# Kernel tuning notes

Hardware: AMD Instinct MI355X
Metric: run time of the kernel (lower is better)

## Reference

```python
import jax, jax.numpy as jnp
import numpy as np

N_NODES = 100_000
N_EDGES = 1_600_000
N_GRAPHS = 1_000
VOCAB = 65
D_IN = 128
D_HID = 128


def setup_inputs() -> dict:
    key = jax.random.key(0)
    ks = jax.random.split(key, 12)
    x = jax.random.randint(ks[0], (N_NODES,), 0, VOCAB)
    edge_index = jax.random.randint(ks[1], (2, N_EDGES), 0, N_NODES)
    batch = jnp.sort(jax.random.randint(ks[2], (N_NODES,), 0, N_GRAPHS))

    def lin(k, fan_in, fan_out):
        bound = 1.0 / np.sqrt(fan_in)
        kw, kb = jax.random.split(k)
        W = jax.random.uniform(kw, (fan_in, fan_out), jnp.float32, -bound, bound)
        b = jax.random.uniform(kb, (fan_out,), jnp.float32, -bound, bound)
        return W, b

    emb = jax.random.normal(ks[3], (VOCAB, D_IN), jnp.float32)
    W1, b1 = lin(ks[4], D_IN, D_HID)
    W2, b2 = lin(ks[5], D_HID, D_HID)
    W3, b3 = lin(ks[6], D_HID, D_HID)
    Wf, bf = lin(ks[7], D_HID, 1)
    return {"x": x, "edge_index": edge_index, "batch": batch, "emb": emb,
            "W1": W1, "b1": b1, "W2": W2, "b2": b2, "W3": W3, "b3": b3,
            "Wf": Wf, "bf": bf}


def gcn_conv(h, W, b, src, dst, n):
    # PyG GCNConv: add self-loops, symmetric normalization D^-1/2 A_hat D^-1/2,
    # transform then aggregate messages at dst.
    h = h @ W                                             # [N, H]
    deg = jnp.zeros((n,), h.dtype).at[dst].add(1.0) + 1.0  # self-loop adds 1
    dinv = jax.lax.rsqrt(deg)                             # [N]
    coef = dinv[src] * dinv[dst]                          # [E]
    agg = jax.ops.segment_sum(h[src] * coef[:, None], dst, num_segments=n)
    return agg + h * (dinv * dinv)[:, None] + b           # self-loop term + bias


def reference(x, edge_index, batch, emb, W1, b1, W2, b2, W3, b3, Wf, bf):
    # Embedding with max_norm=1: renormalize looked-up rows to norm <= 1.
    e = emb[x]                                            # [N, D_IN]
    nrm = jnp.linalg.norm(e, axis=-1, keepdims=True)
    e = e * jnp.minimum(1.0, 1.0 / jnp.maximum(nrm, 1e-7))

    src, dst = edge_index[0], edge_index[1]
    h = jax.nn.relu(gcn_conv(e, W1, b1, src, dst, N_NODES))
    h = jax.nn.relu(gcn_conv(h, W2, b2, src, dst, N_NODES))
    h = jax.nn.relu(gcn_conv(h, W3, b3, src, dst, N_NODES))

    g = jax.ops.segment_max(h, batch, num_segments=N_GRAPHS)  # [G, H]
    return (g @ Wf + bf).ravel()                               # [G]
```

## Files before the change

### kernel.cpp

```cpp
#include <hip/hip_runtime.h>
#include <hip/hip_bf16.h>

#define N_NODES  100000
#define N_EDGES  1600000
#define N_GRAPHS 1000
#define D        128
#define CAP      64
#define NBKT     256
#define N_BUCKETS ((N_NODES + NBKT - 1) / NBKT)
#define HWGS     256
#define EPW      ((N_EDGES + HWGS - 1) / HWGS)

typedef __attribute__((ext_vector_type(8))) short bf16x8;
typedef __attribute__((ext_vector_type(4))) float f32x4;

__device__ inline f32x4 mfma16(bf16x8 a, bf16x8 b, f32x4 c) {
    return __builtin_amdgcn_mfma_f32_16x16x32_bf16(a, b, c, 0, 0, 0);
}

__device__ inline unsigned short f2bf(float f) {
    unsigned u = __float_as_uint(f);
    unsigned r = u + 0x7fffu + ((u >> 16) & 1u);
    return (unsigned short)(r >> 16);
}

__global__ __launch_bounds__(256) void k_hist(const int* __restrict__ dst,
                                              int* __restrict__ bcnt,
                                              int* __restrict__ wgoff,
                                              const float* __restrict__ W1,
                                              const float* __restrict__ W2,
                                              const float* __restrict__ W3,
                                              short* __restrict__ frag) {
    int w = blockIdx.x, t = threadIdx.x;
    if (w >= HWGS) {
        int L = w - HWGS;
        const float* W = (L == 0) ? W1 : (L == 1) ? W2 : W3;
        short* fh = frag + (size_t)L * 32768;
        short* fl = fh + 16384;
        #pragma unroll
        for (int f = 0; f < 8; f++) {
            int id = t + f * 256;
            int lane = id & 63, kb = (id >> 6) & 3, nt = id >> 8;
            int k0 = kb * 32 + (lane >> 4) * 8;
            int n  = nt * 16 + (lane & 15);
            bf16x8 vh, vl;
            #pragma unroll
            for (int j = 0; j < 8; j++) {
                float wv = W[(k0 + j) * 128 + n];
                unsigned short hs = f2bf(wv);
                float hf = __uint_as_float((unsigned)hs << 16);
                vh[j] = (short)hs;
                vl[j] = (short)f2bf(wv - hf);
            }
            *(bf16x8*)&fh[id * 8] = vh;
            *(bf16x8*)&fl[id * 8] = vl;
        }
        return;
    }
    __shared__ int hist[N_BUCKETS];
    for (int b = t; b < N_BUCKETS; b += 256) hist[b] = 0;
    __syncthreads();
    int e0 = w * EPW, e1 = min(e0 + EPW, N_EDGES);
    for (int i = e0 + t; i < e1; i += 256)
        atomicAdd(&hist[dst[i] >> 8], 1);
    __syncthreads();
    for (int b = t; b < N_BUCKETS; b += 256) {
        int h = hist[b];
        wgoff[w * N_BUCKETS + b] = h ? atomicAdd(&bcnt[b], h) : 0;
    }
}

__global__ __launch_bounds__(512) void k_bscan(const int* __restrict__ bcnt,
                                               int* __restrict__ boff) {
    __shared__ int s[512];
    int t = threadIdx.x;
    int v = (t < N_BUCKETS) ? bcnt[t] : 0;
    s[t] = v;
    __syncthreads();
    for (int off = 1; off < 512; off <<= 1) {
        int val = (t >= off) ? s[t - off] : 0;
        __syncthreads();
        s[t] += val;
        __syncthreads();
    }
    if (t < N_BUCKETS) boff[t] = s[t] - v;
    if (t == 0) boff[N_BUCKETS] = N_EDGES;
}

__global__ __launch_bounds__(256) void k_scat(const int* __restrict__ src,
                                              const int* __restrict__ dst,
                                              const int* __restrict__ boff,
                                              const int* __restrict__ wgoff,
                                              int* __restrict__ ep) {
    __shared__ int cnt[N_BUCKETS];
    int t = threadIdx.x, w = blockIdx.x;
    for (int b = t; b < N_BUCKETS; b += 256) cnt[b] = 0;
    __syncthreads();
    int e0 = w * EPW, e1 = min(e0 + EPW, N_EDGES);
    for (int i = e0 + t; i < e1; i += 256) {
        int d = dst[i], b = d >> 8;
        int r = atomicAdd(&cnt[b], 1);
        ep[boff[b] + wgoff[w * N_BUCKETS + b] + r] = (src[i] << 8) | (d & 255);
    }
}

__global__ __launch_bounds__(256) void k_ell(const int* __restrict__ ep,
                                             const int* __restrict__ boff,
                                             int* __restrict__ ell,
                                             int* __restrict__ fill) {
    __shared__ int cnt_s[NBKT];
    __shared__ int ell_s[NBKT * CAP];
    int t = threadIdx.x, b = blockIdx.x;
    int nb0 = b * NBKT;
    int nn = min(NBKT, N_NODES - nb0);
    for (int i = t; i < NBKT; i += 256) cnt_s[i] = 0;
    __syncthreads();
    int e0 = boff[b], e1 = boff[b + 1];
    for (int i = e0 + t; i < e1; i += 256) {
        int e = ep[i];
        int ln = e & 255;
        int r = atomicAdd(&cnt_s[ln], 1);
        if (r < CAP) ell_s[ln * CAP + r] = (int)((unsigned)e >> 8);
    }
    __syncthreads();
    for (int i = t; i < nn * CAP; i += 256)
        ell[(size_t)nb0 * CAP + i] = ell_s[i];
    if (t < nn) fill[nb0 + t] = cnt_s[t];
}

__global__ __launch_bounds__(256) void k_embed(const int* __restrict__ x,
                                               const float* __restrict__ emb,
                                               unsigned short* __restrict__ h,
                                               const int* __restrict__ batch,
                                               int* __restrict__ gstart,
                                               int* __restrict__ gend) {
    int gid = blockIdx.x * 256 + threadIdx.x;
    if (gid < N_NODES) {
        int b = batch[gid];
        if (gid == 0 || batch[gid - 1] != b) gstart[b] = gid;
        if (gid == N_NODES - 1 || batch[gid + 1] != b) gend[b] = gid + 1;
    }
    int n = blockIdx.x * 4 + (threadIdx.x >> 6);
    int lane = threadIdx.x & 63;
    if (n >= N_NODES) return;
    int xi = x[n];
    float2 v = ((const float2*)(emb + (size_t)xi * D))[lane];
    float ss = v.x * v.x + v.y * v.y;
    #pragma unroll
    for (int off = 32; off; off >>= 1) ss += __shfl_xor(ss, off);
    float nrm = sqrtf(ss);
    float scale = fminf(1.0f, 1.0f / fmaxf(nrm, 1e-7f));
    unsigned pk = (unsigned)f2bf(v.x * scale) | ((unsigned)f2bf(v.y * scale) << 16);
    ((unsigned*)(h + (size_t)n * D))[lane] = pk;
}

__global__ __launch_bounds__(256) void k_gemm(const unsigned short* __restrict__ A,
                                              const short* __restrict__ frag,
                                              const int* __restrict__ fill,
                                              unsigned short* __restrict__ Cb) {
    __shared__ short Bf[16384];
    int t = threadIdx.x;
    int w = t >> 6, lane = t & 63;
    int quad = lane >> 4, col = lane & 15;
    size_t r0 = (size_t)blockIdx.x * 128 + w * 32;

    bf16x8 a0[4], a1[4];
    #pragma unroll
    for (int kb = 0; kb < 4; kb++) {
        a0[kb] = *(const bf16x8*)&A[(r0 + col)      * D + kb * 32 + quad * 8];
        a1[kb] = *(const bf16x8*)&A[(r0 + 16 + col) * D + kb * 32 + quad * 8];
    }
    f32x4 acc[2][8];
    #pragma unroll
    for (int r = 0; r < 2; r++)
        #pragma unroll
        for (int n = 0; n < 8; n++) acc[r][n] = (f32x4){0.f, 0.f, 0.f, 0.f};

    #pragma unroll
    for (int half = 0; half < 2; half++) {
        __syncthreads();
        {
            const int4* g4 = (const int4*)(frag + half * 16384);
            int4* l4 = (int4*)Bf;
            #pragma unroll
            for (int i = 0; i < 8; i++) l4[t + i * 256] = g4[t + i * 256];
        }
        __syncthreads();
        #pragma unroll
        for (int kb = 0; kb < 4; kb++)
            #pragma unroll
            for (int nt = 0; nt < 8; nt++) {
                bf16x8 b = *(const bf16x8*)&Bf[((nt * 4 + kb) * 64 + lane) * 8];
                acc[0][nt] = mfma16(a0[kb], b, acc[0][nt]);
                acc[1][nt] = mfma16(a1[kb], b, acc[1][nt]);
            }
    }
    #pragma unroll
    for (int r = 0; r < 2; r++) {
        size_t row = r0 + r * 16 + quad * 4;
        #pragma unroll
        for (int g = 0; g < 4; g++) {
            float dv = (row + g < N_NODES)
                         ? 1.0f / sqrtf((float)fill[row + g] + 1.0f) : 0.f;
            #pragma unroll
            for (int nt = 0; nt < 8; nt++)
                Cb[(row + g) * D + nt * 16 + col] = f2bf(acc[r][nt][g] * dv);
        }
    }
}

__device__ inline void acc8(float* acc, int4 r) {
    unsigned u0 = (unsigned)r.x, u1 = (unsigned)r.y,
             u2 = (unsigned)r.z, u3 = (unsigned)r.w;
    acc[0] += __uint_as_float(u0 << 16);
    acc[1] += __uint_as_float(u0 & 0xffff0000u);
    acc[2] += __uint_as_float(u1 << 16);
    acc[3] += __uint_as_float(u1 & 0xffff0000u);
    acc[4] += __uint_as_float(u2 << 16);
    acc[5] += __uint_as_float(u2 & 0xffff0000u);
    acc[6] += __uint_as_float(u3 << 16);
    acc[7] += __uint_as_float(u3 & 0xffff0000u);
}

#define LOADGRP(R, S, IT)                                                    \
    {                                                                        \
        _Pragma("unroll")                                                    \
        for (int k = 0; k < 4; k++) {                                        \
            int s = __shfl((S), (IT) * 16 + k * 4 + quad);                   \
            R[k] = *(const int4*)&hw2[((unsigned)s << 7) + cOff];            \
        }                                                                    \
    }
#define ACCGRP(A, R)                                                         \
    {                                                                        \
        _Pragma("unroll")                                                    \
        for (int k = 0; k < 4; k++) acc8((A), R[k]);                         \
    }

__global__ __launch_bounds__(256) void k_agg(const unsigned short* __restrict__ hw2,
                                             unsigned short* __restrict__ hout,
                                             const int* __restrict__ fill,
                                             const int* __restrict__ ell,
                                             const float* __restrict__ bias) {
    int w = threadIdx.x >> 6, lane = threadIdx.x & 63;
    int na = blockIdx.x * 8 + w * 2;
    int nb = na + 1;
    if (na >= N_NODES) return;
    int quad = lane >> 4;
    int l16  = lane & 15;
    unsigned cOff = (unsigned)(l16 << 3);

    int fa = __builtin_amdgcn_readfirstlane(fill[na]);
    int fb = __builtin_amdgcn_readfirstlane(fill[nb]);
    int ca = min(fa, CAP), cb = min(fb, CAP);
    int sa = (lane < ca) ? ell[na * CAP + lane] : N_NODES;
    int sb = (lane < cb) ? ell[nb * CAP + lane] : N_NODES;
    int ia = (ca + 15) >> 4; ia += (ia == 0);
    int ib = (cb + 15) >> 4; ib += (ib == 0);

    float accA[8], accB[8];
    #pragma unroll
    for (int c = 0; c < 8; c++) { accA[c] = 0.f; accB[c] = 0.f; }

    int4 A0[4], A1[4], B0[4], B1[4];
    LOADGRP(A0, sa, 0);
    LOADGRP(B0, sb, 0);
    if (1 < ia) LOADGRP(A1, sa, 1);
    ACCGRP(accA, A0);
    if (1 < ib) LOADGRP(B1, sb, 1);
    ACCGRP(accB, B0);
    if (ia > 1 || ib > 1) {
        if (2 < ia) LOADGRP(A0, sa, 2);
        if (1 < ia) ACCGRP(accA, A1);
        if (2 < ib) LOADGRP(B0, sb, 2);
        if (1 < ib) ACCGRP(accB, B1);
        if (ia > 2 || ib > 2) {
            if (3 < ia) LOADGRP(A1, sa, 3);
            if (2 < ia) ACCGRP(accA, A0);
            if (3 < ib) LOADGRP(B1, sb, 3);
            if (2 < ib) ACCGRP(accB, B0);
            if (3 < ia) ACCGRP(accA, A1);
            if (3 < ib) ACCGRP(accB, B1);
        }
    }

    #pragma unroll
    for (int c = 0; c < 8; c++) {
        accA[c] += __shfl_xor(accA[c], 16);
        accA[c] += __shfl_xor(accA[c], 32);
        accB[c] += __shfl_xor(accB[c], 16);
        accB[c] += __shfl_xor(accB[c], 32);
    }
    if (quad < 2) {
        int   n   = quad ? nb : na;
        int   fr  = quad ? fb : fa;
        float* acc = quad ? accB : accA;
        int4 sr = *(const int4*)&hw2[((unsigned)n << 7) + cOff];
        acc8(acc, sr);
        float di = 1.0f / sqrtf((float)fr + 1.0f);
        float4 bA = *(const float4*)&bias[l16 * 8];
        float4 bB = *(const float4*)&bias[l16 * 8 + 4];
        float o[8];
        o[0] = fmaxf(acc[0] * di + bA.x, 0.f);
        o[1] = fmaxf(acc[1] * di + bA.y, 0.f);
        o[2] = fmaxf(acc[2] * di + bA.z, 0.f);
        o[3] = fmaxf(acc[3] * di + bA.w, 0.f);
        o[4] = fmaxf(acc[4] * di + bB.x, 0.f);
        o[5] = fmaxf(acc[5] * di + bB.y, 0.f);
        o[6] = fmaxf(acc[6] * di + bB.z, 0.f);
        o[7] = fmaxf(acc[7] * di + bB.w, 0.f);
        int4 pk;
        pk.x = (int)((unsigned)f2bf(o[0]) | ((unsigned)f2bf(o[1]) << 16));
        pk.y = (int)((unsigned)f2bf(o[2]) | ((unsigned)f2bf(o[3]) << 16));
        pk.z = (int)((unsigned)f2bf(o[4]) | ((unsigned)f2bf(o[5]) << 16));
        pk.w = (int)((unsigned)f2bf(o[6]) | ((unsigned)f2bf(o[7]) << 16));
        *(int4*)&hout[((unsigned)n << 7) + cOff] = pk;
    }
}

__global__ __launch_bounds__(256) void k_pool(const unsigned short* __restrict__ h,
                                              const int* __restrict__ gstart,
                                              const int* __restrict__ gend,
                                              const float* __restrict__ Wf,
                                              const float* __restrict__ bf,
                                              float* __restrict__ out) {
    __shared__ float2 sm[4][64];
    int g = blockIdx.x;
    int w = threadIdx.x >> 6, lane = threadIdx.x & 63;
    int s = gstart[g], e = gend[g];
    float2 m = make_float2(-3.402823466e38f, -3.402823466e38f);
    for (int i = s + w; i < e; i += 4) {
        unsigned u = ((const unsigned*)(h + (size_t)i * D))[lane];
        m.x = fmaxf(m.x, __uint_as_float(u << 16));
        m.y = fmaxf(m.y, __uint_as_float(u & 0xffff0000u));
    }
    sm[w][lane] = m;
    __syncthreads();
    if (w == 0) {
        float2 a = sm[0][lane], b2 = sm[1][lane], c = sm[2][lane], d = sm[3][lane];
        m.x = fmaxf(fmaxf(a.x, b2.x), fmaxf(c.x, d.x));
        m.y = fmaxf(fmaxf(a.y, b2.y), fmaxf(c.y, d.y));
        float2 wf = ((const float2*)Wf)[lane];
        float val = m.x * wf.x + m.y * wf.y;
        #pragma unroll
        for (int off = 32; off; off >>= 1) val += __shfl_xor(val, off);
        if (lane == 0) out[g] = val + bf[0];
    }
}

extern "C" void kernel_launch(void* const* d_in, const int* in_sizes, int n_in,
                              void* d_out, int out_size, void* d_ws, size_t ws_size,
                              hipStream_t stream) {
    const int*   x    = (const int*)d_in[0];
    const int*   ei   = (const int*)d_in[1];
    const int*   batch= (const int*)d_in[2];
    const float* emb  = (const float*)d_in[3];
    const float* W1   = (const float*)d_in[4];
    const float* b1   = (const float*)d_in[5];
    const float* W2   = (const float*)d_in[6];
    const float* b2   = (const float*)d_in[7];
    const float* W3   = (const float*)d_in[8];
    const float* b3   = (const float*)d_in[9];
    const float* Wf   = (const float*)d_in[10];
    const float* bf   = (const float*)d_in[11];
    float* out = (float*)d_out;

    const int* src = ei;
    const int* dst = ei + N_EDGES;

    char* p = (char*)d_ws;
    unsigned short* hAb  = (unsigned short*)p; p += (size_t)(N_NODES + 128) * D * 2;
    unsigned short* hwb  = (unsigned short*)p; p += (size_t)(N_NODES + 128) * D * 2;
    int*            ep   = (int*)hwb;
    int*   fill     = (int*)p;              p += (size_t)N_NODES * 4;
    int*   gbounds  = (int*)p;              p += (size_t)2 * N_GRAPHS * 4;
    int*   ell      = (int*)p;              p += (size_t)N_NODES * CAP * 4;
    int*   wgoff    = (int*)p;              p += (size_t)HWGS * N_BUCKETS * 4;
    int*   bcnt     = (int*)p;              p += (size_t)(N_BUCKETS + 4) * 4;
    int*   boff     = (int*)p;              p += (size_t)(N_BUCKETS + 4) * 4;
    short* wfrag    = (short*)p;            p += (size_t)3 * 32768 * 2;
    (void)p;
    int* gstart = gbounds;
    int* gend   = gbounds + N_GRAPHS;

    hipMemsetAsync(bcnt, 0, (size_t)N_BUCKETS * 4, stream);
    hipMemsetAsync(gbounds, 0x7f, (size_t)2 * N_GRAPHS * 4, stream);

    const int NW = (N_NODES + 3) / 4;
    const int GB = (N_NODES + 127) / 128;
    const int AB = N_NODES / 8;

    k_hist <<<HWGS + 3, 256, 0, stream>>>(dst, bcnt, wgoff, W1, W2, W3, wfrag);
    k_bscan<<<1, 512, 0, stream>>>(bcnt, boff);
    k_scat <<<HWGS, 256, 0, stream>>>(src, dst, boff, wgoff, ep);
    k_ell  <<<N_BUCKETS, 256, 0, stream>>>(ep, boff, ell, fill);

    k_embed<<<NW, 256, 0, stream>>>(x, emb, hAb, batch, gstart, gend);

    k_gemm<<<GB, 256, 0, stream>>>(hAb, wfrag,         fill, hwb);
    k_agg <<<AB, 256, 0, stream>>>(hwb, hAb, fill, ell, b1);
    k_gemm<<<GB, 256, 0, stream>>>(hAb, wfrag + 32768, fill, hwb);
    k_agg <<<AB, 256, 0, stream>>>(hwb, hAb, fill, ell, b2);
    k_gemm<<<GB, 256, 0, stream>>>(hAb, wfrag + 65536, fill, hwb);
    k_agg <<<AB, 256, 0, stream>>>(hwb, hAb, fill, ell, b3);

    k_pool<<<N_GRAPHS, 256, 0, stream>>>(hAb, gstart, gend, Wf, bf, out);
}
```

Before: 413.6 us.

## Fuse embedding lookup into first GEMM and move graph bounds into hist kernel

```diff
diff --git a/kernel.cpp b/kernel.cpp
--- a/kernel.cpp
+++ b/kernel.cpp
@@ -10,6 +10,7 @@
 #define N_BUCKETS ((N_NODES + NBKT - 1) / NBKT)
 #define HWGS     256
 #define EPW      ((N_EDGES + HWGS - 1) / HWGS)
+#define BNDB     ((N_NODES + 255) / 256)
 
 typedef __attribute__((ext_vector_type(8))) short bf16x8;
 typedef __attribute__((ext_vector_type(4))) float f32x4;
@@ -30,8 +31,20 @@
                                               const float* __restrict__ W1,
                                               const float* __restrict__ W2,
                                               const float* __restrict__ W3,
-                                              short* __restrict__ frag) {
+                                              short* __restrict__ frag,
+                                              const int* __restrict__ batch,
+                                              int* __restrict__ gstart,
+                                              int* __restrict__ gend) {
     int w = blockIdx.x, t = threadIdx.x;
+    if (w >= HWGS + 3) {
+        int gid = (w - HWGS - 3) * 256 + t;
+        if (gid < N_NODES) {
+            int b = batch[gid];
+            if (gid == 0 || batch[gid - 1] != b) gstart[b] = gid;
+            if (gid == N_NODES - 1 || batch[gid + 1] != b) gend[b] = gid + 1;
+        }
+        return;
+    }
     if (w >= HWGS) {
         int L = w - HWGS;
         const float* W = (L == 0) ? W1 : (L == 1) ? W2 : W3;
@@ -128,73 +141,25 @@
     if (t < nn) fill[nb0 + t] = cnt_s[t];
 }
 
-__global__ __launch_bounds__(256) void k_embed(const int* __restrict__ x,
-                                               const float* __restrict__ emb,
-                                               unsigned short* __restrict__ h,
-                                               const int* __restrict__ batch,
-                                               int* __restrict__ gstart,
-                                               int* __restrict__ gend) {
-    int gid = blockIdx.x * 256 + threadIdx.x;
-    if (gid < N_NODES) {
-        int b = batch[gid];
-        if (gid == 0 || batch[gid - 1] != b) gstart[b] = gid;
-        if (gid == N_NODES - 1 || batch[gid + 1] != b) gend[b] = gid + 1;
-    }
-    int n = blockIdx.x * 4 + (threadIdx.x >> 6);
-    int lane = threadIdx.x & 63;
-    if (n >= N_NODES) return;
-    int xi = x[n];
-    float2 v = ((const float2*)(emb + (size_t)xi * D))[lane];
-    float ss = v.x * v.x + v.y * v.y;
-    #pragma unroll
-    for (int off = 32; off; off >>= 1) ss += __shfl_xor(ss, off);
-    float nrm = sqrtf(ss);
-    float scale = fminf(1.0f, 1.0f / fmaxf(nrm, 1e-7f));
-    unsigned pk = (unsigned)f2bf(v.x * scale) | ((unsigned)f2bf(v.y * scale) << 16);
-    ((unsigned*)(h + (size_t)n * D))[lane] = pk;
-}
-
-__global__ __launch_bounds__(256) void k_gemm(const unsigned short* __restrict__ A,
-                                              const short* __restrict__ frag,
-                                              const int* __restrict__ fill,
-                                              unsigned short* __restrict__ Cb) {
-    __shared__ short Bf[16384];
-    int t = threadIdx.x;
-    int w = t >> 6, lane = t & 63;
-    int quad = lane >> 4, col = lane & 15;
-    size_t r0 = (size_t)blockIdx.x * 128 + w * 32;
-
-    bf16x8 a0[4], a1[4];
-    #pragma unroll
-    for (int kb = 0; kb < 4; kb++) {
-        a0[kb] = *(const bf16x8*)&A[(r0 + col)      * D + kb * 32 + quad * 8];
-        a1[kb] = *(const bf16x8*)&A[(r0 + 16 + col) * D + kb * 32 + quad * 8];
-    }
-    f32x4 acc[2][8];
-    #pragma unroll
-    for (int r = 0; r < 2; r++)
-        #pragma unroll
-        for (int n = 0; n < 8; n++) acc[r][n] = (f32x4){0.f, 0.f, 0.f, 0.f};
-
-    #pragma unroll
-    for (int half = 0; half < 2; half++) {
-        __syncthreads();
-        {
-            const int4* g4 = (const int4*)(frag + half * 16384);
-            int4* l4 = (int4*)Bf;
-            #pragma unroll
-            for (int i = 0; i < 8; i++) l4[t + i * 256] = g4[t + i * 256];
-        }
-        __syncthreads();
-        #pragma unroll
-        for (int kb = 0; kb < 4; kb++)
-            #pragma unroll
-            for (int nt = 0; nt < 8; nt++) {
-                bf16x8 b = *(const bf16x8*)&Bf[((nt * 4 + kb) * 64 + lane) * 8];
-                acc[0][nt] = mfma16(a0[kb], b, acc[0][nt]);
-                acc[1][nt] = mfma16(a1[kb], b, acc[1][nt]);
-            }
-    }
+__device__ inline void gemm_body(const short* Bh, const short* Bl,
+                                 const bf16x8* a0, const bf16x8* a1,
+                                 f32x4 acc[2][8], int lane) {
+    #pragma unroll
+    for (int kb = 0; kb < 4; kb++)
+        #pragma unroll
+        for (int nt = 0; nt < 8; nt++) {
+            bf16x8 bh = *(const bf16x8*)&Bh[((nt * 4 + kb) * 64 + lane) * 8];
+            bf16x8 bl = *(const bf16x8*)&Bl[((nt * 4 + kb) * 64 + lane) * 8];
+            acc[0][nt] = mfma16(a0[kb], bh, acc[0][nt]);
+            acc[0][nt] = mfma16(a0[kb], bl, acc[0][nt]);
+            acc[1][nt] = mfma16(a1[kb], bh, acc[1][nt]);
+            acc[1][nt] = mfma16(a1[kb], bl, acc[1][nt]);
+        }
+}
+
+__device__ inline void gemm_epilogue(f32x4 acc[2][8], const int* fill,
+                                     unsigned short* Cb, size_t r0,
+                                     int quad, int col) {
     #pragma unroll
     for (int r = 0; r < 2; r++) {
         size_t row = r0 + r * 16 + quad * 4;
@@ -207,6 +172,100 @@
                 Cb[(row + g) * D + nt * 16 + col] = f2bf(acc[r][nt][g] * dv);
         }
     }
+}
+
+__global__ __launch_bounds__(256) void k_gemm1e(const int* __restrict__ x,
+                                                const float* __restrict__ emb,
+                                                const short* __restrict__ frag,
+                                                const int* __restrict__ fill,
+                                                unsigned short* __restrict__ Cb) {
+    __shared__ short Bfrag[2 * 16384];
+    int t = threadIdx.x;
+    {
+        const int4* g4 = (const int4*)frag;
+        int4* l4 = (int4*)Bfrag;
+        #pragma unroll
+        for (int i = 0; i < 16; i++) l4[t + i * 256] = g4[t + i * 256];
+    }
+    int w = t >> 6, lane = t & 63;
+    int quad = lane >> 4, col = lane & 15;
+    size_t r0 = (size_t)blockIdx.x * 128 + w * 32;
+
+    bf16x8 a0[4], a1[4];
+    {
+        size_t ra = r0 + col, rb = r0 + 16 + col;
+        int xa = (ra < N_NODES) ? x[ra] : 0;
+        int xb = (rb < N_NODES) ? x[rb] : 0;
+        float va[32], vb[32];
+        float ssa = 0.f, ssb = 0.f;
+        #pragma unroll
+        for (int kb = 0; kb < 4; kb++) {
+            float4 pa0 = *(const float4*)&emb[(size_t)xa * D + kb * 32 + quad * 8];
+            float4 pa1 = *(const float4*)&emb[(size_t)xa * D + kb * 32 + quad * 8 + 4];
+            float4 pb0 = *(const float4*)&emb[(size_t)xb * D + kb * 32 + quad * 8];
+            float4 pb1 = *(const float4*)&emb[(size_t)xb * D + kb * 32 + quad * 8 + 4];
+            va[kb*8+0]=pa0.x; va[kb*8+1]=pa0.y; va[kb*8+2]=pa0.z; va[kb*8+3]=pa0.w;
+            va[kb*8+4]=pa1.x; va[kb*8+5]=pa1.y; va[kb*8+6]=pa1.z; va[kb*8+7]=pa1.w;
+            vb[kb*8+0]=pb0.x; vb[kb*8+1]=pb0.y; vb[kb*8+2]=pb0.z; vb[kb*8+3]=pb0.w;
+            vb[kb*8+4]=pb1.x; vb[kb*8+5]=pb1.y; vb[kb*8+6]=pb1.z; vb[kb*8+7]=pb1.w;
+            #pragma unroll
+            for (int j = 0; j < 8; j++) { ssa += va[kb*8+j]*va[kb*8+j];
+                                          ssb += vb[kb*8+j]*vb[kb*8+j]; }
+        }
+        ssa += __shfl_xor(ssa, 16); ssa += __shfl_xor(ssa, 32);
+        ssb += __shfl_xor(ssb, 16); ssb += __shfl_xor(ssb, 32);
+        float sca = fminf(1.0f, 1.0f / fmaxf(sqrtf(ssa), 1e-7f));
+        float scb = fminf(1.0f, 1.0f / fmaxf(sqrtf(ssb), 1e-7f));
+        #pragma unroll
+        for (int kb = 0; kb < 4; kb++) {
+            bf16x8 fa, fb;
+            #pragma unroll
+            for (int j = 0; j < 8; j++) {
+                fa[j] = (short)f2bf(va[kb*8+j] * sca);
+                fb[j] = (short)f2bf(vb[kb*8+j] * scb);
+            }
+            a0[kb] = fa; a1[kb] = fb;
+        }
+    }
+    f32x4 acc[2][8];
+    #pragma unroll
+    for (int r = 0; r < 2; r++)
+        #pragma unroll
+        for (int n = 0; n < 8; n++) acc[r][n] = (f32x4){0.f, 0.f, 0.f, 0.f};
+    __syncthreads();
+    gemm_body(Bfrag, Bfrag + 16384, a0, a1, acc, lane);
+    gemm_epilogue(acc, fill, Cb, r0, quad, col);
+}
+
+__global__ __launch_bounds__(256) void k_gemm(const unsigned short* __restrict__ A,
+                                              const short* __restrict__ frag,
+                                              const int* __restrict__ fill,
+                                              unsigned short* __restrict__ Cb) {
+    __shared__ short Bfrag[2 * 16384];
+    int t = threadIdx.x;
+    {
+        const int4* g4 = (const int4*)frag;
+        int4* l4 = (int4*)Bfrag;
+        #pragma unroll
+        for (int i = 0; i < 16; i++) l4[t + i * 256] = g4[t + i * 256];
+    }
+    __syncthreads();
+    int w = t >> 6, lane = t & 63;
+    int quad = lane >> 4, col = lane & 15;
+    size_t r0 = (size_t)blockIdx.x * 128 + w * 32;
+    bf16x8 a0[4], a1[4];
+    #pragma unroll
+    for (int kb = 0; kb < 4; kb++) {
+        a0[kb] = *(const bf16x8*)&A[(r0 + col)      * D + kb * 32 + quad * 8];
+        a1[kb] = *(const bf16x8*)&A[(r0 + 16 + col) * D + kb * 32 + quad * 8];
+    }
+    f32x4 acc[2][8];
+    #pragma unroll
+    for (int r = 0; r < 2; r++)
+        #pragma unroll
+        for (int n = 0; n < 8; n++) acc[r][n] = (f32x4){0.f, 0.f, 0.f, 0.f};
+    gemm_body(Bfrag, Bfrag + 16384, a0, a1, acc, lane);
+    gemm_epilogue(acc, fill, Cb, r0, quad, col);
 }
 
 __device__ inline void acc8(float* acc, int4 r) {
@@ -385,19 +444,17 @@
     hipMemsetAsync(bcnt, 0, (size_t)N_BUCKETS * 4, stream);
     hipMemsetAsync(gbounds, 0x7f, (size_t)2 * N_GRAPHS * 4, stream);
 
-    const int NW = (N_NODES + 3) / 4;
     const int GB = (N_NODES + 127) / 128;
     const int AB = N_NODES / 8;
 
-    k_hist <<<HWGS + 3, 256, 0, stream>>>(dst, bcnt, wgoff, W1, W2, W3, wfrag);
+    k_hist <<<HWGS + 3 + BNDB, 256, 0, stream>>>(dst, bcnt, wgoff, W1, W2, W3,
+                                                 wfrag, batch, gstart, gend);
     k_bscan<<<1, 512, 0, stream>>>(bcnt, boff);
     k_scat <<<HWGS, 256, 0, stream>>>(src, dst, boff, wgoff, ep);
     k_ell  <<<N_BUCKETS, 256, 0, stream>>>(ep, boff, ell, fill);
 
-    k_embed<<<NW, 256, 0, stream>>>(x, emb, hAb, batch, gstart, gend);
-
-    k_gemm<<<GB, 256, 0, stream>>>(hAb, wfrag,         fill, hwb);
-    k_agg <<<AB, 256, 0, stream>>>(hwb, hAb, fill, ell, b1);
+    k_gemm1e<<<GB, 256, 0, stream>>>(x, emb, wfrag, fill, hwb);
+    k_agg   <<<AB, 256, 0, stream>>>(hwb, hAb, fill, ell, b1);
     k_gemm<<<GB, 256, 0, stream>>>(hAb, wfrag + 32768, fill, hwb);
     k_agg <<<AB, 256, 0, stream>>>(hwb, hAb, fill, ell, b2);
     k_gemm<<<GB, 256, 0, stream>>>(hAb, wfrag + 65536, fill, hwb);
```

Result: faster. 375.8 us (-9.1%).
